# Performance work log

Measured on AMD Instinct MI355X. Metric: run time of the kernel, lower is better.

Reference implementation:

```python
import jax, jax.numpy as jnp
import numpy as np

B, C, H, W = 4, 256, 64, 64
N = H * W


def _conv1x1(x, w, b):
    # x: [B,C,H,W], w: [O,C], b: [O]  (1x1 conv == per-pixel linear)
    return jnp.einsum('bchw,oc->bohw', x, w) + b[None, :, None, None]


def setup_inputs() -> dict:
    key = jax.random.key(0)
    ks = jax.random.split(key, 11)
    s = 1.0 / np.sqrt(C)
    x = jax.random.normal(ks[0], (B, C, H, W), dtype=jnp.float32)
    mkw = lambda k: jax.random.normal(k, (C, C), dtype=jnp.float32) * s
    mkb = lambda k: jax.random.normal(k, (C,), dtype=jnp.float32) * 0.01
    return {
        'x': x,
        'w_teta': mkw(ks[1]), 'b_teta': mkb(ks[2]),
        'w_fi': mkw(ks[3]), 'b_fi': mkb(ks[4]),
        'w_gi': mkw(ks[5]), 'b_gi': mkb(ks[6]),
        'w_o1': mkw(ks[7]), 'b_o1': mkb(ks[8]),
        'w_o2': mkw(ks[9]), 'b_o2': mkb(ks[10]),
    }


def reference(x, w_teta, b_teta, w_fi, b_fi, w_gi, b_gi, w_o1, b_o1, w_o2, b_o2):
    b, c, h, w = x.shape
    n = h * w
    # 1x1 projections, flattened to [B,C,N]
    x1 = _conv1x1(x, w_teta, b_teta).reshape(b, c, n)
    x2 = _conv1x1(x, w_fi, b_fi).reshape(b, c, n)
    x3 = _conv1x1(x, w_gi, b_gi).reshape(b, c, n)
    # NOTE: original uses .view (memory reinterpretation), NOT transpose
    x1 = x1.reshape(b, n, c)
    x3 = x3.reshape(b, n, c)
    scores = jnp.einsum('bnc,bcm->bnm', x1, x2)      # [B,N,N]
    s_row = jax.nn.softmax(scores, axis=2)
    s_col = jax.nn.softmax(scores, axis=1)
    y1 = jnp.einsum('bnm,bmc->bnc', s_row, x3)       # [B,N,C]
    y2 = jnp.einsum('bnm,bmc->bnc', s_col, x3)
    # transpose(1,2) then view -> contiguous transpose + reshape
    y1 = jnp.swapaxes(y1, 1, 2).reshape(b, c, h, w)
    y2 = jnp.swapaxes(y2, 1, 2).reshape(b, c, h, w)
    o1 = _conv1x1(y1, w_o1, b_o1)
    o2 = _conv1x1(y2, w_o2, b_o2)
    xx = jnp.concatenate([x, x], axis=1)             # [B,2C,H,W]
    agg = jnp.concatenate([o1, o2], axis=1)
    return jax.nn.relu(xx + agg)
```

## Files before the change

### kernel.cpp

```cpp
#include <hip/hip_runtime.h>

#define BB   4
#define CC   256
#define NPIX 4096
#define AST2 40
#define YST  72

typedef __attribute__((ext_vector_type(8)))  short bf16x8;
typedef __attribute__((ext_vector_type(8)))  _Float16 f16x8;
typedef __attribute__((ext_vector_type(4)))  short short4v;
typedef __attribute__((ext_vector_type(16))) float f32x16;

__device__ __forceinline__ short f2h(float f) {
    _Float16 h = (_Float16)f;
    return __builtin_bit_cast(short, h);
}
__device__ __forceinline__ int cdrow(int r, int l5) {
    return (r & 3) + 8 * (r >> 2) + 4 * l5;
}
__device__ __forceinline__ short s_enc(float v) {
    float c = fmaxf(fminf(v, 127.9f), -127.9f);
    return (short)__float2int_rn(c * 256.0f);
}
__device__ __forceinline__ float s_dec(short v) {
    return (float)v * (1.0f / 256.0f);
}

__device__ __forceinline__ void mfma_core_f16(
    const short* __restrict__ A, const short* __restrict__ B, f32x16 acc[2][2])
{
    __shared__ short LA[128 * AST2], LB[128 * AST2];
    const int t = threadIdx.x;
    const int lane = t & 63, w = t >> 6;
    const int l31 = lane & 31, l5 = lane >> 5;
    const int nq = (w & 1) * 64, mq = (w >> 1) * 64;
    const int sr = t >> 1;
    const int sk = (t & 1) * 16;
    const size_t gs = (size_t)sr * 256 + sk;
    const int ls = sr * AST2 + sk;

    bf16x8 rA0 = *(const bf16x8*)(A + gs);
    bf16x8 rA1 = *(const bf16x8*)(A + gs + 8);
    bf16x8 rB0 = *(const bf16x8*)(B + gs);
    bf16x8 rB1 = *(const bf16x8*)(B + gs + 8);

    for (int k0 = 0; k0 < 256; k0 += 32) {
        __syncthreads();
        *(bf16x8*)&LA[ls]     = rA0;
        *(bf16x8*)&LA[ls + 8] = rA1;
        *(bf16x8*)&LB[ls]     = rB0;
        *(bf16x8*)&LB[ls + 8] = rB1;
        __syncthreads();
        if (k0 + 32 < 256) {
            size_t g = gs + k0 + 32;
            rA0 = *(const bf16x8*)(A + g);
            rA1 = *(const bf16x8*)(A + g + 8);
            rB0 = *(const bf16x8*)(B + g);
            rB1 = *(const bf16x8*)(B + g + 8);
        }
#pragma unroll
        for (int ks = 0; ks < 2; ks++) {
            f16x8 a[2], b[2];
#pragma unroll
            for (int s = 0; s < 2; s++) {
                a[s] = *(const f16x8*)&LA[(nq + s * 32 + l31) * AST2 + ks * 16 + l5 * 8];
                b[s] = *(const f16x8*)&LB[(mq + s * 32 + l31) * AST2 + ks * 16 + l5 * 8];
            }
#pragma unroll
            for (int s = 0; s < 2; s++)
#pragma unroll
                for (int u = 0; u < 2; u++)
                    acc[s][u] = __builtin_amdgcn_mfma_f32_32x32x16_f16(a[s], b[u], acc[s][u], 0, 0, 0);
        }
    }
}


__global__ __launch_bounds__(256) void pack_w5(
    const float* __restrict__ w0, const float* __restrict__ w1,
    const float* __restrict__ w2, const float* __restrict__ w3,
    const float* __restrict__ w4, short* __restrict__ wall)
{
    int which = blockIdx.y;
    const float* w = which == 0 ? w0 : which == 1 ? w1 : which == 2 ? w2
                   : which == 3 ? w3 : w4;
    int idx = blockIdx.x * 1024 + threadIdx.x * 4;
    float4 v = *(const float4*)(w + idx);
    short4v h;
    h.x = f2h(v.x); h.y = f2h(v.y); h.z = f2h(v.z); h.w = f2h(v.w);
    *(short4v*)(wall + which * 65536 + idx) = h;
}

__global__ __launch_bounds__(256) void pack_t_f16(
    const float* __restrict__ in, short* __restrict__ o16)
{
    __shared__ short T[32][36];
    const int b  = blockIdx.z;
    const int n0 = blockIdx.x * 32;
    const int c0 = blockIdx.y * 32;
    const float* src = in + (size_t)b * CC * NPIX;
    const int t = threadIdx.x;
    const int r = t >> 3, q = t & 7;
    float4 v = *(const float4*)(src + (size_t)(c0 + r) * NPIX + n0 + q * 4);
    T[q * 4 + 0][r] = f2h(v.x);
    T[q * 4 + 1][r] = f2h(v.y);
    T[q * 4 + 2][r] = f2h(v.z);
    T[q * 4 + 3][r] = f2h(v.w);
    __syncthreads();
    short4v o;
    o.x = T[r][q * 4 + 0];
    o.y = T[r][q * 4 + 1];
    o.z = T[r][q * 4 + 2];
    o.w = T[r][q * 4 + 3];
    size_t oo = (size_t)b * CC * NPIX + (size_t)(n0 + r) * 256 + c0 + q * 4;
    *(short4v*)(o16 + oo) = o;
}

__global__ __launch_bounds__(256) void tr16_cn(
    const short* __restrict__ in, short* __restrict__ outp)
{
    __shared__ short T[32][33];
    const int b  = blockIdx.z;
    const int n0 = blockIdx.x * 32;
    const int c0 = blockIdx.y * 32;
    const short* src = in + (size_t)b * CC * NPIX;
    short* dst = outp + (size_t)b * CC * NPIX;
    const int t = threadIdx.x;
    const int r = t >> 3, q = t & 7;
    short4v v = *(const short4v*)(src + (size_t)(c0 + r) * NPIX + n0 + q * 4);
    T[q * 4 + 0][r] = v.x;
    T[q * 4 + 1][r] = v.y;
    T[q * 4 + 2][r] = v.z;
    T[q * 4 + 3][r] = v.w;
    __syncthreads();
    short4v o;
    o.x = T[r][q * 4 + 0];
    o.y = T[r][q * 4 + 1];
    o.z = T[r][q * 4 + 2];
    o.w = T[r][q * 4 + 3];
    *(short4v*)(dst + (size_t)(n0 + r) * 256 + c0 + q * 4) = o;
}

__global__ __launch_bounds__(256) void packVt_bf(
    const short* __restrict__ x3f, short* __restrict__ Vt)
{
    __shared__ short T[32][33];
    const int b  = blockIdx.z;
    const int m0 = blockIdx.x * 32;
    const int c0 = blockIdx.y * 32;
    const short* in = x3f + (size_t)b * CC * NPIX;
    short* out = Vt + (size_t)b * CC * NPIX;
    const int t = threadIdx.x;
    const int r = t >> 3, q = t & 7;
    short4v v = *(const short4v*)(in + (size_t)(m0 + r) * CC + c0 + q * 4);
    T[q * 4 + 0][r] = v.x;
    T[q * 4 + 1][r] = v.y;
    T[q * 4 + 2][r] = v.z;
    T[q * 4 + 3][r] = v.w;
    __syncthreads();
    short4v o;
    o.x = T[r][q * 4 + 0];
    o.y = T[r][q * 4 + 1];
    o.z = T[r][q * 4 + 2];
    o.w = T[r][q * 4 + 3];
    *(short4v*)(out + (size_t)(c0 + r) * NPIX + m0 + q * 4) = o;
}


__global__ __launch_bounds__(256) void proj_mfma(
    const short* __restrict__ wpf, const short* __restrict__ xtf,
    const float* __restrict__ b_teta, const float* __restrict__ b_fi,
    const float* __restrict__ b_gi,
    short* __restrict__ x1f, short* __restrict__ x2f, short* __restrict__ x3f)
{
    const int z = blockIdx.z, p = z >> 2, b = z & 3;
    const int n0 = blockIdx.x * 128, c0 = blockIdx.y * 128;
    const size_t CN = (size_t)CC * NPIX;
    const short* Ah = wpf + p * 65536 + c0 * 256;
    const short* Bh = xtf + (size_t)b * CN + (size_t)n0 * 256;
    const float* bias = p == 0 ? b_teta : p == 1 ? b_fi : b_gi;
    short* dst = p == 0 ? x1f : p == 1 ? x2f : x3f;

    f32x16 acc[2][2] = {};
    mfma_core_f16(Ah, Bh, acc);

    const int t = threadIdx.x, lane = t & 63, w = t >> 6;
    const int l31 = lane & 31, l5 = lane >> 5;
    const int aq = (w & 1) * 64, bq = (w >> 1) * 64;
#pragma unroll
    for (int s = 0; s < 2; s++)
#pragma unroll
        for (int u = 0; u < 2; u++)
#pragma unroll
            for (int r = 0; r < 16; r++) {
                int c = c0 + aq + s * 32 + cdrow(r, l5);
                int n = n0 + bq + u * 32 + l31;
                float v = acc[s][u][r] + bias[c];
                size_t o = (size_t)b * CN + (size_t)c * NPIX + n;
                dst[o] = f2h(v);
            }
}

__global__ __launch_bounds__(256) void scores_mfma(
    const short* __restrict__ x1f, const short* __restrict__ x2tf,
    short* __restrict__ S16, float* __restrict__ pm, float* __restrict__ pl)
{
    const int m0 = blockIdx.x * 128, n0 = blockIdx.y * 128;
    f32x16 acc[2][2] = {};
    mfma_core_f16(x1f + (size_t)n0 * 256, x2tf + (size_t)m0 * 256, acc);

    const int t = threadIdx.x, lane = t & 63, w = t >> 6;
    const int l31 = lane & 31, l5 = lane >> 5;
    const int aq = (w & 1) * 64, bq = (w >> 1) * 64;
#pragma unroll
    for (int s = 0; s < 2; s++)
#pragma unroll
        for (int u = 0; u < 2; u++)
#pragma unroll
            for (int r = 0; r < 16; r++) {
                int n = n0 + aq + s * 32 + cdrow(r, l5);
                int m = m0 + bq + u * 32 + l31;
                S16[(size_t)n * NPIX + m] = s_enc(acc[s][u][r]);
            }

    const int member = w & 1;
#pragma unroll
    for (int u = 0; u < 2; u++) {
        float vmax = -1e30f;
#pragma unroll
        for (int s = 0; s < 2; s++)
#pragma unroll
            for (int r = 0; r < 16; r++) vmax = fmaxf(vmax, acc[s][u][r]);
        float vsum = 0.0f;
#pragma unroll
        for (int s = 0; s < 2; s++)
#pragma unroll
            for (int r = 0; r < 16; r++) vsum += __expf(acc[s][u][r] - vmax);
        float vmax2 = __shfl_xor(vmax, 32, 64);
        float vsum2 = __shfl_xor(vsum, 32, 64);
        float mc = fmaxf(vmax, vmax2);
        float sc = vsum * __expf(vmax - mc) + vsum2 * __expf(vmax2 - mc);
        if (l5 == 0) {
            size_t pidx = (size_t)(blockIdx.y * 2 + member) * NPIX + m0 + bq + u * 32 + l31;
            pm[pidx] = mc;
            pl[pidx] = sc;
        }
    }
}

__global__ __launch_bounds__(256) void out_mfma(
    const short* __restrict__ wof,
    const float* __restrict__ b_o1, const float* __restrict__ b_o2,
    const short* __restrict__ Yp,
    const float* __restrict__ x, float* __restrict__ out, int b)
{
    __shared__ short LA[128 * AST2], LB[128 * AST2];
    const size_t CN_ = (size_t)NPIX * CC;
    const int ch0 = blockIdx.y * 128;
    const int pix0 = blockIdx.x * 128;
    const int mode = ch0 < 256 ? 0 : 1;
    const short* W = wof + mode * 65536 + (size_t)(ch0 & 255) * 256;
    const short* Yq = Yp + (size_t)mode * 4 * CN_;
    const float* bias = mode == 0 ? b_o1 : b_o2;

    const int t = threadIdx.x, lane = t & 63, w = t >> 6;
    const int l31 = lane & 31, l5 = lane >> 5;
    const int nq = (w & 1) * 64, mq = (w >> 1) * 64;
    const int sr = t >> 1;
    const int sk = (t & 1) * 16;
    const size_t gsA = (size_t)sr * 256 + sk;
    const size_t gsB = (size_t)(pix0 + sr) * 256 + sk;
    const int ls = sr * AST2 + sk;

    f32x16 acc[2][2] = {};

    bf16x8 rA0 = *(const bf16x8*)(W + gsA);
    bf16x8 rA1 = *(const bf16x8*)(W + gsA + 8);
    f16x8 rB0, rB1;
    {
        rB0 = *(const f16x8*)(Yq + gsB);
        rB1 = *(const f16x8*)(Yq + gsB + 8);
#pragma unroll
        for (int q = 1; q < 4; q++) {
            rB0 = rB0 + *(const f16x8*)(Yq + (size_t)q * CN_ + gsB);
            rB1 = rB1 + *(const f16x8*)(Yq + (size_t)q * CN_ + gsB + 8);
        }
    }

    for (int k0 = 0; k0 < 256; k0 += 32) {
        __syncthreads();
        *(bf16x8*)&LA[ls]    = rA0;
        *(bf16x8*)&LA[ls + 8] = rA1;
        *(f16x8*)&LB[ls]     = rB0;
        *(f16x8*)&LB[ls + 8] = rB1;
        __syncthreads();
        if (k0 + 32 < 256) {
            size_t gA = gsA + k0 + 32;
            size_t gB = gsB + k0 + 32;
            rA0 = *(const bf16x8*)(W + gA);
            rA1 = *(const bf16x8*)(W + gA + 8);
            rB0 = *(const f16x8*)(Yq + gB);
            rB1 = *(const f16x8*)(Yq + gB + 8);
#pragma unroll
            for (int q = 1; q < 4; q++) {
                rB0 = rB0 + *(const f16x8*)(Yq + (size_t)q * CN_ + gB);
                rB1 = rB1 + *(const f16x8*)(Yq + (size_t)q * CN_ + gB + 8);
            }
        }
#pragma unroll
        for (int ks = 0; ks < 2; ks++) {
            f16x8 a[2], bb[2];
#pragma unroll
            for (int s = 0; s < 2; s++) {
                a[s]  = *(const f16x8*)&LA[(nq + s * 32 + l31) * AST2 + ks * 16 + l5 * 8];
                bb[s] = *(const f16x8*)&LB[(mq + s * 32 + l31) * AST2 + ks * 16 + l5 * 8];
            }
#pragma unroll
            for (int s = 0; s < 2; s++)
#pragma unroll
                for (int u = 0; u < 2; u++)
                    acc[s][u] = __builtin_amdgcn_mfma_f32_32x32x16_f16(a[s], bb[u], acc[s][u], 0, 0, 0);
        }
    }

    const int aq = (w & 1) * 64, bq = (w >> 1) * 64;
#pragma unroll
    for (int s = 0; s < 2; s++)
#pragma unroll
        for (int u = 0; u < 2; u++)
#pragma unroll
            for (int r = 0; r < 16; r++) {
                int ch = ch0 + aq + s * 32 + cdrow(r, l5);
                int pix = pix0 + bq + u * 32 + l31;
                int chm = ch & 255;
                float v = acc[s][u][r] + bias[chm] +
                          x[((size_t)b * CC + chm) * NPIX + pix];
                out[((size_t)b * 2 * CC + ch) * NPIX + pix] = fmaxf(v, 0.0f);
            }
}

__global__ __launch_bounds__(256) void stats16_kernel(
    const short* __restrict__ S16,
    const float* __restrict__ pm, const float* __restrict__ pl,
    float* __restrict__ cm, float* __restrict__ cli,
    float* __restrict__ rm, float* __restrict__ rli)
{
    __shared__ float sm[4][64], sl[4][64];
    __shared__ float red[4];
    const int t = threadIdx.x;
    if (blockIdx.x < 64) {
        const int cl = t & 63, ch = t >> 6;
        const int col = blockIdx.x * 64 + cl;
        float m = -1e30f, l = 0.0f;
        for (int i = ch * 16; i < ch * 16 + 16; i++) {
            float m2 = pm[(size_t)i * NPIX + col];
            float l2 = pl[(size_t)i * NPIX + col];
            float mn = fmaxf(m, m2);
            l = l * __expf(m - mn) + l2 * __expf(m2 - mn);
            m = mn;
        }
        sm[ch][cl] = m;
        sl[ch][cl] = l;
        __syncthreads();
        if (ch == 0) {
#pragma unroll
            for (int j = 1; j < 4; j++) {
                float m2 = sm[j][cl], l2 = sl[j][cl];
                float mn = fmaxf(m, m2);
                l = l * __expf(m - mn) + l2 * __expf(m2 - mn);
                m = mn;
            }
            cm[col]  = m;
            cli[col] = 1.0f / l;
        }
    } else {
        const int row = blockIdx.x - 64;
        const short* sp = S16 + (size_t)row * NPIX;
        const int w = t >> 6, lane = t & 63;
        float s4[16];
#pragma unroll
        for (int i = 0; i < 4; i++) {
            short4v v = *(const short4v*)(sp + (i * 256 + t) * 4);
            s4[i * 4 + 0] = s_dec(v.x);
            s4[i * 4 + 1] = s_dec(v.y);
            s4[i * 4 + 2] = s_dec(v.z);
            s4[i * 4 + 3] = s_dec(v.w);
        }
        float m = -1e30f;
#pragma unroll
        for (int i = 0; i < 16; i++) m = fmaxf(m, s4[i]);
        for (int off = 32; off; off >>= 1) m = fmaxf(m, __shfl_xor(m, off, 64));
        if (lane == 0) red[w] = m;
        __syncthreads();
        m = fmaxf(fmaxf(red[0], red[1]), fmaxf(red[2], red[3]));
        __syncthreads();
        float sum = 0.0f;
#pragma unroll
        for (int i = 0; i < 16; i++) sum += __expf(s4[i] - m);
        for (int off = 32; off; off >>= 1) sum += __shfl_xor(sum, off, 64);
        if (lane == 0) red[w] = sum;
        __syncthreads();
        if (t == 0) {
            rm[row]  = m;
            rli[row] = 1.0f / (red[0] + red[1] + red[2] + red[3]);
        }
    }
}

__device__ __forceinline__ void compute_ph(
    const short4v sv[4], int mode, int mg,
    const float* __restrict__ cmv, const float* __restrict__ cliv,
    float mrow, float lrow, short4v ph[4])
{
    if (mode == 0) {
#pragma unroll
        for (int i = 0; i < 4; i++) {
            ph[i].x = f2h(__expf(s_dec(sv[i].x) - mrow) * lrow);
            ph[i].y = f2h(__expf(s_dec(sv[i].y) - mrow) * lrow);
            ph[i].z = f2h(__expf(s_dec(sv[i].z) - mrow) * lrow);
            ph[i].w = f2h(__expf(s_dec(sv[i].w) - mrow) * lrow);
        }
    } else {
#pragma unroll
        for (int i = 0; i < 4; i++) {
            float4 cm4 = *(const float4*)(cmv + mg + i * 4);
            float4 cl4 = *(const float4*)(cliv + mg + i * 4);
            ph[i].x = f2h(__expf(s_dec(sv[i].x) - cm4.x) * cl4.x);
            ph[i].y = f2h(__expf(s_dec(sv[i].y) - cm4.y) * cl4.y);
            ph[i].z = f2h(__expf(s_dec(sv[i].z) - cm4.z) * cl4.z);
            ph[i].w = f2h(__expf(s_dec(sv[i].w) - cm4.w) * cl4.w);
        }
    }
}

__global__ __launch_bounds__(256) void pv_kernel(
    const short* __restrict__ S16, const short* __restrict__ Vt,
    const float* __restrict__ rmv, const float* __restrict__ rliv,
    const float* __restrict__ cmv, const float* __restrict__ cliv,
    short* __restrict__ Yp)
{
    __shared__ short LA[64 * YST];
    __shared__ short LB[256 * YST];
    const int mode = blockIdx.z, kq = blockIdx.y;
    const int n0 = blockIdx.x * 64;
    const int kbase = kq * 1024;

    const int t = threadIdx.x, lane = t & 63, w = t >> 6;
    const int l31 = lane & 31, l5 = lane >> 5;
    const int nst = (w & 1) * 32, cb = (w >> 1) * 128;
    const int ar = t >> 2;
    const int ak = (t & 3) * 16;

    const float mrow = rmv[n0 + ar];
    const float lrow = rliv[n0 + ar];
    const short* sp = S16 + (size_t)(n0 + ar) * NPIX + kbase + ak;

    short4v svA[4], svB[4];
    bf16x8 pbA[8], pbB[8];
#pragma unroll
    for (int i = 0; i < 4; i++) {
        svA[i] = *(const short4v*)(sp + i * 4);
        svB[i] = *(const short4v*)(sp + 64 + i * 4);
    }
#pragma unroll
    for (int i = 0; i < 4; i++) {
        const short* bp0 = Vt + (size_t)(i * 64 + ar) * NPIX + kbase + ak;
        pbA[2 * i]     = *(const bf16x8*)bp0;
        pbA[2 * i + 1] = *(const bf16x8*)(bp0 + 8);
        pbB[2 * i]     = *(const bf16x8*)(bp0 + 64);
        pbB[2 * i + 1] = *(const bf16x8*)(bp0 + 72);
    }

    f32x16 acc[4] = {};
    for (int sx = 0; sx < 8; sx++) {
        const int s = sx * 2;
        {
            short4v ph[4];
            compute_ph(svA, mode, kbase + s * 64 + ak, cmv, cliv, mrow, lrow, ph);
            __syncthreads();
#pragma unroll
            for (int i = 0; i < 4; i++)
                *(short4v*)&LA[ar * YST + ak + i * 4] = ph[i];
#pragma unroll
            for (int i = 0; i < 4; i++) {
                *(bf16x8*)&LB[(i * 64 + ar) * YST + ak]     = pbA[2 * i];
                *(bf16x8*)&LB[(i * 64 + ar) * YST + ak + 8] = pbA[2 * i + 1];
            }
            __syncthreads();
            if (s + 2 < 16) {
                const short* spn = sp + (s + 2) * 64;
#pragma unroll
                for (int i = 0; i < 4; i++)
                    svA[i] = *(const short4v*)(spn + i * 4);
                int kg = kbase + (s + 2) * 64 + ak;
#pragma unroll
                for (int i = 0; i < 4; i++) {
                    const short* bp = Vt + (size_t)(i * 64 + ar) * NPIX + kg;
                    pbA[2 * i]     = *(const bf16x8*)bp;
                    pbA[2 * i + 1] = *(const bf16x8*)(bp + 8);
                }
            }
#pragma unroll
            for (int kc = 0; kc < 4; kc++) {
                f16x8 af = *(const f16x8*)&LA[(nst + l31) * YST + kc * 16 + l5 * 8];
#pragma unroll
                for (int u = 0; u < 4; u++) {
                    f16x8 bf = *(const f16x8*)&LB[(cb + u * 32 + l31) * YST + kc * 16 + l5 * 8];
                    acc[u] = __builtin_amdgcn_mfma_f32_32x32x16_f16(af, bf, acc[u], 0, 0, 0);
                }
            }
        }
        {
            short4v ph[4];
            compute_ph(svB, mode, kbase + (s + 1) * 64 + ak, cmv, cliv, mrow, lrow, ph);
            __syncthreads();
#pragma unroll
            for (int i = 0; i < 4; i++)
                *(short4v*)&LA[ar * YST + ak + i * 4] = ph[i];
#pragma unroll
            for (int i = 0; i < 4; i++) {
                *(bf16x8*)&LB[(i * 64 + ar) * YST + ak]     = pbB[2 * i];
                *(bf16x8*)&LB[(i * 64 + ar) * YST + ak + 8] = pbB[2 * i + 1];
            }
            __syncthreads();
            if (s + 3 < 16) {
                const short* spn = sp + (s + 3) * 64;
#pragma unroll
                for (int i = 0; i < 4; i++)
                    svB[i] = *(const short4v*)(spn + i * 4);
                int kg = kbase + (s + 3) * 64 + ak;
#pragma unroll
                for (int i = 0; i < 4; i++) {
                    const short* bp = Vt + (size_t)(i * 64 + ar) * NPIX + kg;
                    pbB[2 * i]     = *(const bf16x8*)bp;
                    pbB[2 * i + 1] = *(const bf16x8*)(bp + 8);
                }
            }
#pragma unroll
            for (int kc = 0; kc < 4; kc++) {
                f16x8 af = *(const f16x8*)&LA[(nst + l31) * YST + kc * 16 + l5 * 8];
#pragma unroll
                for (int u = 0; u < 4; u++) {
                    f16x8 bf = *(const f16x8*)&LB[(cb + u * 32 + l31) * YST + kc * 16 + l5 * 8];
                    acc[u] = __builtin_amdgcn_mfma_f32_32x32x16_f16(af, bf, acc[u], 0, 0, 0);
                }
            }
        }
    }

    short* Yo = Yp + (size_t)(mode * 4 + kq) * ((size_t)NPIX * CC);
#pragma unroll
    for (int u = 0; u < 4; u++)
#pragma unroll
        for (int r = 0; r < 16; r++) {
            int rr = cdrow(r, l5);
            Yo[(size_t)(n0 + nst + rr) * CC + cb + u * 32 + l31] = f2h(acc[u][r]);
        }
}

extern "C" void kernel_launch(void* const* d_in, const int* in_sizes, int n_in,
                              void* d_out, int out_size, void* d_ws, size_t ws_size,
                              hipStream_t stream)
{
    (void)in_sizes; (void)n_in; (void)out_size; (void)ws_size;
    const float* x      = (const float*)d_in[0];
    const float* w_teta = (const float*)d_in[1];
    const float* b_teta = (const float*)d_in[2];
    const float* w_fi   = (const float*)d_in[3];
    const float* b_fi   = (const float*)d_in[4];
    const float* w_gi   = (const float*)d_in[5];
    const float* b_gi   = (const float*)d_in[6];
    const float* w_o1   = (const float*)d_in[7];
    const float* b_o1   = (const float*)d_in[8];
    const float* w_o2   = (const float*)d_in[9];
    const float* b_o2   = (const float*)d_in[10];
    float* out = (float*)d_out;

    const size_t CN = (size_t)CC * NPIX;
    const size_t NN = (size_t)NPIX * NPIX;
    short* wsp   = (short*)d_ws;
    short* S16   = wsp;
    short* Yp    = S16 + NN;
    short* x1f   = Yp + 16 * CN;
    short* x2tf  = x1f + BB * CN;
    short* Vtb   = x2tf + BB * CN;
    float* cm    = (float*)(Vtb + BB * CN);
    float* cli   = cm + NPIX;
    float* rm    = cli + NPIX;
    float* rli   = rm + NPIX;
    float* pm    = rli + NPIX;
    float* pl    = pm + 64 * NPIX;
    short* wall  = (short*)(pl + 64 * NPIX);
    short* wpf   = wall;
    short* wof   = wall + 3 * 65536;
    short* xtf  = Yp;
    short* x2f  = S16;
    short* x3f  = S16 + BB * CN;

    dim3 blk(256);
    pack_w5<<<dim3(64, 5), blk, 0, stream>>>(w_teta, w_fi, w_gi, w_o1, w_o2, wall);
    pack_t_f16<<<dim3(128, 8, 4), blk, 0, stream>>>(x, xtf);

    proj_mfma<<<dim3(32, 2, 12), blk, 0, stream>>>(
        wpf, xtf, b_teta, b_fi, b_gi, x1f, x2f, x3f);

    tr16_cn<<<dim3(128, 8, 4), blk, 0, stream>>>(x2f, x2tf);
    packVt_bf<<<dim3(128, 8, 4), blk, 0, stream>>>(x3f, Vtb);

    for (int b = 0; b < BB; b++) {
        scores_mfma<<<dim3(32, 32), blk, 0, stream>>>(
            x1f + b * CN, x2tf + b * CN, S16, pm, pl);
        stats16_kernel<<<dim3(64 + NPIX), blk, 0, stream>>>(
            S16, pm, pl, cm, cli, rm, rli);
        pv_kernel<<<dim3(64, 4, 2), blk, 0, stream>>>(
            S16, Vtb + b * CN, rm, rli, cm, cli, Yp);
        out_mfma<<<dim3(32, 4), blk, 0, stream>>>(
            wof, b_o1, b_o2, Yp, x, out, b);
    }
}
```

Before: 455.3 us.

## Enlarge scores GEMM tile to 256x128 with register-prefetched LDS staging

The scores kernel now computes a 256x128 output tile per block instead of 128x128, with each wave holding a 4x2 grid of 32x32 MFMA accumulators. Global loads for the next K-slice are prefetched into registers while MFMAs run on the current LDS slice. The grid is halved in y, and the stats kernel's partial-max/sum reduction shrinks from 64 to 32 row-partials to match. The bigger tile reuses the B operand more, but it doubles accumulator registers and launches fewer blocks (512 per batch), which can hurt occupancy.

```diff
diff --git a/kernel.cpp b/kernel.cpp
--- a/kernel.cpp
+++ b/kernel.cpp
@@ -201,39 +201,92 @@
             }
 }
 
-__global__ __launch_bounds__(256) void scores_mfma(
+__global__ __launch_bounds__(256, 2) void scores_mfma(
     const short* __restrict__ x1f, const short* __restrict__ x2tf,
     short* __restrict__ S16, float* __restrict__ pm, float* __restrict__ pl)
 {
-    const int m0 = blockIdx.x * 128, n0 = blockIdx.y * 128;
-    f32x16 acc[2][2] = {};
-    mfma_core_f16(x1f + (size_t)n0 * 256, x2tf + (size_t)m0 * 256, acc);
+    __shared__ short LA[256 * AST2];
+    __shared__ short LB[128 * AST2];
+    const int m0 = blockIdx.x * 128, n0 = blockIdx.y * 256;
+    const short* A = x1f + (size_t)n0 * 256;
+    const short* B = x2tf + (size_t)m0 * 256;
 
     const int t = threadIdx.x, lane = t & 63, w = t >> 6;
     const int l31 = lane & 31, l5 = lane >> 5;
-    const int aq = (w & 1) * 64, bq = (w >> 1) * 64;
-#pragma unroll
-    for (int s = 0; s < 2; s++)
+    const int h = w & 1, g = w >> 1;
+
+    const size_t gsA = (size_t)t * 256;
+    const int lsA = t * AST2;
+    const int srB = t >> 1, skB = (t & 1) * 16;
+    const size_t gsB = (size_t)srB * 256 + skB;
+    const int lsB = srB * AST2 + skB;
+
+    bf16x8 rA0 = *(const bf16x8*)(A + gsA);
+    bf16x8 rA1 = *(const bf16x8*)(A + gsA + 8);
+    bf16x8 rA2 = *(const bf16x8*)(A + gsA + 16);
+    bf16x8 rA3 = *(const bf16x8*)(A + gsA + 24);
+    bf16x8 rB0 = *(const bf16x8*)(B + gsB);
+    bf16x8 rB1 = *(const bf16x8*)(B + gsB + 8);
+
+    f32x16 acc[4][2] = {};
+
+    for (int k0 = 0; k0 < 256; k0 += 32) {
+        __syncthreads();
+        *(bf16x8*)&LA[lsA]      = rA0;
+        *(bf16x8*)&LA[lsA + 8]  = rA1;
+        *(bf16x8*)&LA[lsA + 16] = rA2;
+        *(bf16x8*)&LA[lsA + 24] = rA3;
+        *(bf16x8*)&LB[lsB]      = rB0;
+        *(bf16x8*)&LB[lsB + 8]  = rB1;
+        __syncthreads();
+        if (k0 + 32 < 256) {
+            size_t gA = gsA + k0 + 32;
+            size_t gB = gsB + k0 + 32;
+            rA0 = *(const bf16x8*)(A + gA);
+            rA1 = *(const bf16x8*)(A + gA + 8);
+            rA2 = *(const bf16x8*)(A + gA + 16);
+            rA3 = *(const bf16x8*)(A + gA + 24);
+            rB0 = *(const bf16x8*)(B + gB);
+            rB1 = *(const bf16x8*)(B + gB + 8);
+        }
+#pragma unroll
+        for (int ks = 0; ks < 2; ks++) {
+            f16x8 a[4], b[2];
+#pragma unroll
+            for (int s = 0; s < 4; s++)
+                a[s] = *(const f16x8*)&LA[(h * 128 + s * 32 + l31) * AST2 + ks * 16 + l5 * 8];
+#pragma unroll
+            for (int u = 0; u < 2; u++)
+                b[u] = *(const f16x8*)&LB[(g * 64 + u * 32 + l31) * AST2 + ks * 16 + l5 * 8];
+#pragma unroll
+            for (int s = 0; s < 4; s++)
+#pragma unroll
+                for (int u = 0; u < 2; u++)
+                    acc[s][u] = __builtin_amdgcn_mfma_f32_32x32x16_f16(a[s], b[u], acc[s][u], 0, 0, 0);
+        }
+    }
+
+#pragma unroll
+    for (int s = 0; s < 4; s++)
 #pragma unroll
         for (int u = 0; u < 2; u++)
 #pragma unroll
             for (int r = 0; r < 16; r++) {
-                int n = n0 + aq + s * 32 + cdrow(r, l5);
-                int m = m0 + bq + u * 32 + l31;
+                int n = n0 + h * 128 + s * 32 + cdrow(r, l5);
+                int m = m0 + g * 64 + u * 32 + l31;
                 S16[(size_t)n * NPIX + m] = s_enc(acc[s][u][r]);
             }
 
-    const int member = w & 1;
 #pragma unroll
     for (int u = 0; u < 2; u++) {
         float vmax = -1e30f;
 #pragma unroll
-        for (int s = 0; s < 2; s++)
+        for (int s = 0; s < 4; s++)
 #pragma unroll
             for (int r = 0; r < 16; r++) vmax = fmaxf(vmax, acc[s][u][r]);
         float vsum = 0.0f;
 #pragma unroll
-        for (int s = 0; s < 2; s++)
+        for (int s = 0; s < 4; s++)
 #pragma unroll
             for (int r = 0; r < 16; r++) vsum += __expf(acc[s][u][r] - vmax);
         float vmax2 = __shfl_xor(vmax, 32, 64);
@@ -241,7 +294,7 @@
         float mc = fmaxf(vmax, vmax2);
         float sc = vsum * __expf(vmax - mc) + vsum2 * __expf(vmax2 - mc);
         if (l5 == 0) {
-            size_t pidx = (size_t)(blockIdx.y * 2 + member) * NPIX + m0 + bq + u * 32 + l31;
+            size_t pidx = (size_t)(blockIdx.y * 2 + h) * NPIX + m0 + g * 64 + u * 32 + l31;
             pm[pidx] = mc;
             pl[pidx] = sc;
         }
@@ -352,7 +405,7 @@
         const int cl = t & 63, ch = t >> 6;
         const int col = blockIdx.x * 64 + cl;
         float m = -1e30f, l = 0.0f;
-        for (int i = ch * 16; i < ch * 16 + 16; i++) {
+        for (int i = ch * 8; i < ch * 8 + 8; i++) {
             float m2 = pm[(size_t)i * NPIX + col];
             float l2 = pl[(size_t)i * NPIX + col];
             float mn = fmaxf(m, m2);
@@ -608,7 +661,7 @@
     packVt_bf<<<dim3(128, 8, 4), blk, 0, stream>>>(x3f, Vtb);
 
     for (int b = 0; b < BB; b++) {
-        scores_mfma<<<dim3(32, 32), blk, 0, stream>>>(
+        scores_mfma<<<dim3(32, 16), blk, 0, stream>>>(
             x1f + b * CN, x2tf + b * CN, S16, pm, pl);
         stats16_kernel<<<dim3(64 + NPIX), blk, 0, stream>>>(
             S16, pm, pl, cm, cli, rm, rli);
```

After: 448.9 us. About the same (-1.4%).
